# Optimization experiments

Measured on AMD Instinct MI355X. Metric: run time of the kernel, lower is better.

## Reference

```python
import math
import jax, jax.numpy as jnp
import numpy as np

B, L, ENC_IN, TFEAT = 32, 1024, 21, 4
DM, EXP = 256, 2
DI = DM * EXP            # 512 d_inner
DST = 64                 # d_state (= configs.d_ff in this repo)
HD = 64                  # headdim
NH = DI // HD            # 8 heads
DC = 4                   # d_conv
NL = 4                   # n_layers
PRED = 192
CO = 21
Q = 64                   # SSD chunk length
DIP = 2 * DI + 2 * DST + NH    # in_proj out dim (z, xBC, dt)
CONVD = DI + 2 * DST           # depthwise-conv channels


def silu(x):
    return x * jax.nn.sigmoid(x)


def positional_embedding(l, d):
    pe = np.zeros((l, d), np.float32)
    pos = np.arange(l, dtype=np.float32)[:, None]
    div = np.exp(np.arange(0, d, 2, dtype=np.float32) * (-math.log(10000.0) / d))
    pe[:, 0::2] = np.sin(pos * div)
    pe[:, 1::2] = np.cos(pos * div)
    return jnp.asarray(pe)


def layernorm(x, g, b):
    m = jnp.mean(x, -1, keepdims=True)
    v = jnp.mean((x - m) ** 2, -1, keepdims=True)
    return (x - m) * jax.lax.rsqrt(v + 1e-5) * g + b


def segsum(x):
    # x: (..., T) -> (..., T, T); out[i,j] = sum_{j<k<=i} x[k], -inf above diagonal
    T = x.shape[-1]
    xx = jnp.broadcast_to(x[..., :, None], (*x.shape, T))
    m1 = jnp.tril(jnp.ones((T, T), bool), -1)
    xs = jnp.cumsum(jnp.where(m1, xx, 0.0), axis=-2)
    m2 = jnp.tril(jnp.ones((T, T), bool), 0)
    return jnp.where(m2, xs, -jnp.inf)


def ssd(X, A, Bm, Cm):
    # chunked SSD (Mamba2). X: (b,l,h,p) = x*dt; A: (b,l,h) = dt*(-exp(A_log)); B,C: (b,l,n)
    b, l, h, p = X.shape
    c = l // Q
    Xc = X.reshape(b, c, Q, h, p)
    Ac = A.reshape(b, c, Q, h).transpose(0, 3, 1, 2)      # (b,h,c,q)
    Bc = Bm.reshape(b, c, Q, -1)
    Cc = Cm.reshape(b, c, Q, -1)
    Acum = jnp.cumsum(Ac, -1)                              # (b,h,c,q)
    Lmat = jnp.exp(segsum(Ac))                             # (b,h,c,q,q)
    Y_diag = jnp.einsum('bcqn,bcsn,bhcqs,bcshp->bcqhp', Cc, Bc, Lmat, Xc)
    decay_states = jnp.exp(Acum[..., -1:] - Acum)          # (b,h,c,q)
    states = jnp.einsum('bcqn,bhcq,bcqhp->bchpn', Bc, decay_states, Xc)
    states = jnp.concatenate([jnp.zeros_like(states[:, :1]), states], axis=1)  # (b,c+1,h,p,n)
    decay_chunk = jnp.exp(segsum(jnp.pad(Acum[..., -1], ((0, 0), (0, 0), (1, 0)))))  # (b,h,c+1,c+1)
    new_states = jnp.einsum('bhzc,bchpn->bzhpn', decay_chunk, states)
    states = new_states[:, :-1]                            # (b,c,h,p,n) entering each chunk
    sdo = jnp.exp(Acum)                                    # (b,h,c,q)
    Y_off = jnp.einsum('bcqn,bchpn,bhcq->bcqhp', Cc, states, sdo)
    return (Y_diag + Y_off).reshape(b, l, h, p)


def mamba2(x, Wi, cw, cb, dtb, Alog, Dp, gw, Wo):
    b, l, _ = x.shape
    zxbcdt = x @ Wi.T                                      # (b,l,DIP)
    z = zxbcdt[..., :DI]
    xBC = zxbcdt[..., DI:DI + CONVD]
    dt = zxbcdt[..., DI + CONVD:]
    # causal depthwise conv (kernel DC) + SiLU
    xp = jnp.pad(xBC, ((0, 0), (DC - 1, 0), (0, 0)))
    xBC = silu(sum(xp[:, k:k + l, :] * cw[:, k] for k in range(DC)) + cb)
    xs = xBC[..., :DI].reshape(b, l, NH, HD)
    Bm = xBC[..., DI:DI + DST]
    Cm = xBC[..., DI + DST:]
    dt = jax.nn.softplus(dt + dtb)                         # (b,l,NH)
    A = -jnp.exp(Alog)                                     # (NH,)
    y = ssd(xs * dt[..., None], dt * A, Bm, Cm) + xs * Dp[:, None]
    y = y.reshape(b, l, DI)
    y = y * silu(z)                                        # gated RMSNorm
    y = y * jax.lax.rsqrt(jnp.mean(y * y, -1, keepdims=True) + 1e-5) * gw
    return y @ Wo.T


def setup_inputs():
    key = jax.random.key(0)
    ks = jax.random.split(key, 16)
    x_enc = jax.random.normal(ks[0], (B, L, ENC_IN), jnp.float32)
    x_mark_enc = jax.random.normal(ks[1], (B, L, TFEAT), jnp.float32)
    x_dec = jax.random.normal(ks[2], (B, 240, ENC_IN), jnp.float32)
    x_mark_dec = jax.random.normal(ks[3], (B, 240, TFEAT), jnp.float32)
    token_w = jax.random.normal(ks[4], (DM, ENC_IN, 3), jnp.float32) * 0.1
    temb_w = jax.random.normal(ks[5], (DM, TFEAT), jnp.float32) * 0.1
    ln_g = jnp.ones((NL, DM), jnp.float32)
    ln_b = jnp.zeros((NL, DM), jnp.float32)
    in_proj_w = jax.random.normal(ks[6], (NL, DIP, DM), jnp.float32) * (DM ** -0.5)
    conv_w = jax.random.normal(ks[7], (NL, CONVD, DC), jnp.float32) * 0.2
    conv_b = jnp.zeros((NL, CONVD), jnp.float32)
    dt_bias = jax.random.normal(ks[8], (NL, NH), jnp.float32) * 0.5
    A_log = jnp.log(jax.random.uniform(ks[9], (NL, NH), jnp.float32, 1.0, 16.0))
    Dskip = jnp.ones((NL, NH), jnp.float32)
    gnorm_w = jnp.ones((NL, DI), jnp.float32)
    out_proj_w = jax.random.normal(ks[10], (NL, DM, DI), jnp.float32) * (DI ** -0.5)
    head_w = jax.random.normal(ks[11], (CO, DM), jnp.float32) * (DM ** -0.5)
    return dict(x_enc=x_enc, x_mark_enc=x_mark_enc, x_dec=x_dec, x_mark_dec=x_mark_dec,
                token_w=token_w, temb_w=temb_w, ln_g=ln_g, ln_b=ln_b,
                in_proj_w=in_proj_w, conv_w=conv_w, conv_b=conv_b, dt_bias=dt_bias,
                A_log=A_log, Dskip=Dskip, gnorm_w=gnorm_w, out_proj_w=out_proj_w,
                head_w=head_w)


def reference(x_enc, x_mark_enc, x_dec, x_mark_dec, token_w, temb_w, ln_g, ln_b,
              in_proj_w, conv_w, conv_b, dt_bias, A_log, Dskip, gnorm_w, out_proj_w, head_w):
    # instance normalization (detached stats)
    mean = jax.lax.stop_gradient(jnp.mean(x_enc, 1, keepdims=True))
    xz = x_enc - mean
    std = jax.lax.stop_gradient(jnp.sqrt(jnp.var(xz, axis=1, keepdims=True) + 1e-5))
    xz = xz / std
    l = xz.shape[1]
    # token embedding: circular-pad Conv1d(enc_in->d_model, k=3)
    xpad = jnp.pad(xz, ((0, 0), (1, 1), (0, 0)), mode='wrap')
    tok = sum(jnp.einsum('blc,dc->bld', xpad[:, k:k + l], token_w[:, :, k]) for k in range(3))
    h = tok + positional_embedding(l, DM)[None] + x_mark_enc @ temb_w.T
    for i in range(NL):
        y = mamba2(h, in_proj_w[i], conv_w[i], conv_b[i], dt_bias[i], A_log[i],
                   Dskip[i], gnorm_w[i], out_proj_w[i])
        h = layernorm(h + y, ln_g[i], ln_b[i])
    out = h @ head_w.T
    out = out * std + mean
    return out[:, -PRED:, :]
```

## Files before the change

### kernel.cpp

```cpp
#include <hip/hip_runtime.h>
#include <hip/hip_bf16.h>


typedef unsigned short ushort_t;
typedef unsigned int uint_t;
typedef __attribute__((ext_vector_type(8))) short short8;
typedef __attribute__((ext_vector_type(4))) float f32x4;
typedef __attribute__((ext_vector_type(4))) ushort_t ushort4_t;

__device__ __forceinline__ float b2f(ushort_t u) {
    uint_t v = ((uint_t)u) << 16;
    return __builtin_bit_cast(float, v);
}
__device__ __forceinline__ ushort_t f2b(float f) {
    uint_t u = __builtin_bit_cast(uint_t, f);
    uint_t r = (u + 0x7FFFu + ((u >> 16) & 1u)) >> 16;
    return (ushort_t)r;
}
__device__ __forceinline__ uint_t cvt_pk2(float a, float b) {
    uint_t r;
    asm("v_cvt_pk_bf16_f32 %0, %1, %2" : "=v"(r) : "v"(a), "v"(b));
    return r;
}
__device__ __forceinline__ float silu_f(float x) {
    return x / (1.f + __expf(-x));
}
__device__ __forceinline__ void gl_lds16(const ushort_t* g, ushort_t* l) {
    __builtin_amdgcn_global_load_lds(
        (const __attribute__((address_space(1))) unsigned int*)g,
        (__attribute__((address_space(3))) unsigned int*)l, 16, 0, 0);
}

__global__ __launch_bounds__(256) void cvt_pad_ip(const float* __restrict__ in,
        ushort_t* __restrict__ out) {
    int i = blockIdx.x * 256 + threadIdx.x;
    if (i >= 4 * 1280 * 256) return;
    int layer = i / (1280 * 256);
    int rem = i - layer * 1280 * 256;
    int n = rem >> 8, k = rem & 255;
    out[i] = (n < 1160) ? f2b(in[(size_t)layer * 1160 * 256 + n * 256 + k]) : (ushort_t)0;
}
__global__ __launch_bounds__(256) void cvt_wop(const float* __restrict__ in,
        const float* __restrict__ gw, ushort_t* __restrict__ out) {
    int i = blockIdx.x * 256 + threadIdx.x;
    int layer = i >> 17;
    int c = i & 511;
    out[i] = f2b(in[i] * gw[layer * 512 + c]);
}
__global__ __launch_bounds__(256) void cvt_convw(const float* __restrict__ in,
        float* __restrict__ out) {
    int i = blockIdx.x * 256 + threadIdx.x;
    if (i >= 10240) return;
    int layer = i / 2560;
    int rem = i - layer * 2560;
    int k = rem / 640, ch = rem - k * 640;
    out[i] = in[layer * 2560 + ch * 4 + k];
}

__global__ __launch_bounds__(256) void pe_kernel(float* __restrict__ pe) {
    int l = blockIdx.x, d = threadIdx.x;
    float div = __expf((float)(d & ~1) * (-9.210340371976184f / 256.0f));
    float arg = (float)l * div;
    pe[l * 256 + d] = (d & 1) ? cosf(arg) : sinf(arg);
}

__global__ __launch_bounds__(256) void stats_kernel(const float* __restrict__ xe,
        float* __restrict__ meanb, float* __restrict__ stdb, float* __restrict__ rstdb) {
    int bi = blockIdx.x;
    int b = bi / 21, c = bi - b * 21;
    int tid = threadIdx.x;
    float s = 0.f, s2 = 0.f;
    for (int l = tid; l < 1024; l += 256) {
        float v = xe[(b * 1024 + l) * 21 + c];
        s += v; s2 += v * v;
    }
    __shared__ float r1[4], r2[4];
    for (int o = 32; o > 0; o >>= 1) { s += __shfl_down(s, o, 64); s2 += __shfl_down(s2, o, 64); }
    if ((tid & 63) == 0) { r1[tid >> 6] = s; r2[tid >> 6] = s2; }
    __syncthreads();
    if (tid == 0) {
        float S = r1[0] + r1[1] + r1[2] + r1[3];
        float S2 = r2[0] + r2[1] + r2[2] + r2[3];
        float m = S * (1.f / 1024.f);
        float var = S2 * (1.f / 1024.f) - m * m;
        float sd = sqrtf(var + 1e-5f);
        meanb[bi] = m; stdb[bi] = sd; rstdb[bi] = 1.f / sd;
    }
}

__global__ __launch_bounds__(256) void embed3_kernel(const float* __restrict__ xe,
        const float* __restrict__ xm, const float* __restrict__ tokw,
        const float* __restrict__ tembw, const float* __restrict__ pe,
        const float* __restrict__ meanb, const float* __restrict__ rstdb,
        float* __restrict__ h, ushort_t* __restrict__ hbf) {
    int blk = blockIdx.x;
    int b = blk >> 4, t = blk & 15;
    int l0 = t * 64;
    int tid = threadIdx.x;
    __shared__ float xw[66][22];
    __shared__ float xmw[64][4];
    __shared__ float mn[21], rs[21];
    if (tid < 21) { mn[tid] = meanb[b * 21 + tid]; rs[tid] = rstdb[b * 21 + tid]; }
    float twr[63];
    {
        const float* tp = tokw + tid * 63;
        #pragma unroll
        for (int i = 0; i < 63; i++) twr[i] = tp[i];
    }
    float tbr[4];
    #pragma unroll
    for (int k = 0; k < 4; k++) tbr[k] = tembw[tid * 4 + k];
    __syncthreads();
    for (int i = tid; i < 1386; i += 256) {
        int row = i / 21, c = i - row * 21;
        int gl = (l0 - 1 + row + 1024) & 1023;
        xw[row][c] = (xe[(size_t)(b * 1024 + gl) * 21 + c] - mn[c]) * rs[c];
    }
    {
        int row = tid >> 2, c = tid & 3;
        xmw[row][c] = xm[(size_t)(b * 1024 + l0 + row) * 4 + c];
    }
    __syncthreads();
    int d = tid;
    float acc2 = 0.f, acc1 = 0.f;
    for (int r = 0; r < 66; r++) {
        float s0 = 0.f, s1 = 0.f, s2 = 0.f;
        #pragma unroll
        for (int c = 0; c < 21; c++) {
            float xv = xw[r][c];
            s0 += xv * twr[c * 3 + 0];
            s1 += xv * twr[c * 3 + 1];
            s2 += xv * twr[c * 3 + 2];
        }
        if (r >= 2) {
            int li = r - 2;
            float acc = acc2 + s2 + pe[(size_t)(l0 + li) * 256 + d];
            #pragma unroll
            for (int k = 0; k < 4; k++) acc += xmw[li][k] * tbr[k];
            size_t o = (size_t)(b * 1024 + l0 + li) * 256 + d;
            h[o] = acc;
            hbf[o] = f2b(acc);
        }
        acc2 = acc1 + s1;
        acc1 = s0;
    }
}

template<int KDIM>
__device__ __forceinline__ void gemm128_main(const ushort_t* __restrict__ Ab,
        const ushort_t* __restrict__ Wb, ushort_t* sA, ushort_t* sW,
        f32x4 (&acc)[16], int m0, int n0) {
    int tid = threadIdx.x;
    int w = tid >> 6, lane = tid & 63;
    int wm = w >> 1, wn = w & 1;
    int rr = lane & 15, quad = lane >> 4;
    int srow0 = w * 32 + (lane >> 2);
    int skk = (lane & 3) * 8;
    int sl0 = w * 1024 + lane * 8;
    for (int k0 = 0; k0 < KDIM; k0 += 64) {
        __syncthreads();
        #pragma unroll
        for (int p = 0; p < 2; p++) {
            #pragma unroll
            for (int j = 0; j < 2; j++) {
                int row = srow0 + j * 16;
                int koff = k0 + p * 32 + skk;
                gl_lds16(Ab + (size_t)(m0 + row) * KDIM + koff, &sA[p * 4096 + sl0 + j * 512]);
                gl_lds16(Wb + (size_t)(n0 + row) * KDIM + koff, &sW[p * 4096 + sl0 + j * 512]);
            }
        }
        __syncthreads();
        #pragma unroll
        for (int p = 0; p < 2; p++) {
            short8 a[4], b[4];
            #pragma unroll
            for (int i = 0; i < 4; i++)
                a[i] = *(const short8*)&sA[p * 4096 + (wm * 64 + i * 16 + rr) * 32 + quad * 8];
            #pragma unroll
            for (int j = 0; j < 4; j++)
                b[j] = *(const short8*)&sW[p * 4096 + (wn * 64 + j * 16 + rr) * 32 + quad * 8];
            #pragma unroll
            for (int i = 0; i < 4; i++)
                #pragma unroll
                for (int j = 0; j < 4; j++)
                    acc[i * 4 + j] = __builtin_amdgcn_mfma_f32_16x16x32_bf16(a[i], b[j], acc[i * 4 + j], 0, 0, 0);
        }
    }
}

__global__ __launch_bounds__(256) void gemm_ip(const ushort_t* __restrict__ A,
        const ushort_t* __restrict__ W, ushort_t* __restrict__ zbuf,
        ushort_t* __restrict__ xbuf) {
    int g = blockIdx.x;
    int xcd = g & 7, s = g >> 3;
    int sq = s / 10;
    int tn = s - sq * 10;
    int tm = (sq << 3) | xcd;
    int m0 = tm * 128, n0 = tn * 128;
    __shared__ ushort_t sA[8192], sW[8192];
    f32x4 acc[16];
    #pragma unroll
    for (int i = 0; i < 16; i++) acc[i] = (f32x4){0.f, 0.f, 0.f, 0.f};
    gemm128_main<256>(A, W, sA, sW, acc, m0, n0);
    int lane = threadIdx.x & 63, w = threadIdx.x >> 6;
    int wm = w >> 1, wn = w & 1;
    int rr = lane & 15, quad = lane >> 4;
    #pragma unroll
    for (int i = 0; i < 4; i++) {
        int mrow = m0 + wm * 64 + i * 16 + quad * 4;
        #pragma unroll
        for (int j = 0; j < 4; j++) {
            int n = n0 + wn * 64 + j * 16 + rr;
            uint_t u01 = cvt_pk2(acc[i * 4 + j][0], acc[i * 4 + j][1]);
            uint_t u23 = cvt_pk2(acc[i * 4 + j][2], acc[i * 4 + j][3]);
            ushort_t vs[4] = {(ushort_t)u01, (ushort_t)(u01 >> 16),
                              (ushort_t)u23, (ushort_t)(u23 >> 16)};
            #pragma unroll
            for (int r2 = 0; r2 < 4; r2++) {
                if (n < 512) zbuf[(size_t)(mrow + r2) * 512 + n] = vs[r2];
                else if (n < 1160) xbuf[(size_t)(mrow + r2) * 704 + (n - 512)] = vs[r2];
            }
        }
    }
}

__global__ __launch_bounds__(256) void gemm_og(const ushort_t* __restrict__ Yb,
        const ushort_t* __restrict__ Zb, const ushort_t* __restrict__ Wb,
        float* __restrict__ h, ushort_t* __restrict__ hbf,
        const float* __restrict__ lng, const float* __restrict__ lnb) {
    int m0 = blockIdx.x * 64;
    int tid = threadIdx.x;
    int w = tid >> 6, lane = tid & 63;
    int wm = w >> 1, wn = w & 1;
    int rr = lane & 15, quad = lane >> 4;
    __shared__ ushort_t sA[4096];
    __shared__ ushort_t sW[16384];
    __shared__ float gssq[64];
    __shared__ float rsum[64][2], rssq[64][2];

    int arow = tid >> 2;
    int akq = (tid & 3) * 16;
    const ushort_t* yrow = Yb + (size_t)(m0 + arow) * 512 + akq;
    const ushort_t* zrow = Zb + (size_t)(m0 + arow) * 512 + akq;
    ushort_t* adst = &sA[((tid & 3) >> 1) * 2048 + arow * 32 + (tid & 1) * 16];

    f32x4 acc[2][8];
    #pragma unroll
    for (int i = 0; i < 2; i++)
        #pragma unroll
        for (int j = 0; j < 8; j++) acc[i][j] = (f32x4){0.f, 0.f, 0.f, 0.f};
    float ssqr = 0.f;

    short8 y0 = *(const short8*)(yrow);
    short8 y1 = *(const short8*)(yrow + 8);
    short8 z0 = *(const short8*)(zrow);
    short8 z1 = *(const short8*)(zrow + 8);

    for (int k0 = 0; k0 < 512; k0 += 64) {
        __syncthreads();
        short8 ga, gb;
        {
            uint_t* gau = (uint_t*)&ga;
            uint_t* gbu = (uint_t*)&gb;
            #pragma unroll
            for (int jj = 0; jj < 8; jj += 2) {
                float g0 = b2f(((ushort_t*)&y0)[jj]) * silu_f(b2f(((ushort_t*)&z0)[jj]));
                float g1 = b2f(((ushort_t*)&y0)[jj + 1]) * silu_f(b2f(((ushort_t*)&z0)[jj + 1]));
                ssqr += g0 * g0 + g1 * g1;
                gau[jj >> 1] = cvt_pk2(g0, g1);
            }
            #pragma unroll
            for (int jj = 0; jj < 8; jj += 2) {
                float g0 = b2f(((ushort_t*)&y1)[jj]) * silu_f(b2f(((ushort_t*)&z1)[jj]));
                float g1 = b2f(((ushort_t*)&y1)[jj + 1]) * silu_f(b2f(((ushort_t*)&z1)[jj + 1]));
                ssqr += g0 * g0 + g1 * g1;
                gbu[jj >> 1] = cvt_pk2(g0, g1);
            }
        }
        *(short8*)adst = ga;
        *(short8*)(adst + 8) = gb;
        if (k0 + 64 < 512) {
            y0 = *(const short8*)(yrow + k0 + 64);
            y1 = *(const short8*)(yrow + k0 + 72);
            z0 = *(const short8*)(zrow + k0 + 64);
            z1 = *(const short8*)(zrow + k0 + 72);
        }
        #pragma unroll
        for (int p = 0; p < 2; p++) {
            #pragma unroll
            for (int j = 0; j < 4; j++)
                gl_lds16(Wb + (size_t)(w * 64 + j * 16 + (lane >> 2)) * 512
                             + k0 + p * 32 + (lane & 3) * 8,
                         &sW[p * 8192 + w * 2048 + j * 512 + lane * 8]);
        }
        __syncthreads();
        #pragma unroll
        for (int p = 0; p < 2; p++) {
            short8 a[2], b[8];
            #pragma unroll
            for (int i = 0; i < 2; i++)
                a[i] = *(const short8*)&sA[p * 2048 + (wm * 32 + i * 16 + rr) * 32 + quad * 8];
            #pragma unroll
            for (int j = 0; j < 8; j++)
                b[j] = *(const short8*)&sW[p * 8192 + (wn * 128 + j * 16 + rr) * 32 + quad * 8];
            #pragma unroll
            for (int i = 0; i < 2; i++)
                #pragma unroll
                for (int j = 0; j < 8; j++)
                    acc[i][j] = __builtin_amdgcn_mfma_f32_16x16x32_bf16(a[i], b[j], acc[i][j], 0, 0, 0);
        }
    }

    ssqr += __shfl_xor(ssqr, 1, 64);
    ssqr += __shfl_xor(ssqr, 2, 64);
    if ((tid & 3) == 0) gssq[arow] = ssqr;
    __syncthreads();

    float gl[8], bl[8];
    #pragma unroll
    for (int j = 0; j < 8; j++) {
        int col = wn * 128 + j * 16 + rr;
        gl[j] = lng[col]; bl[j] = lnb[col];
    }
    #pragma unroll
    for (int i = 0; i < 2; i++) {
        #pragma unroll
        for (int r2 = 0; r2 < 4; r2++) {
            int rowl = wm * 32 + i * 16 + quad * 4 + r2;
            float rmsv = rsqrtf(gssq[rowl] * (1.f / 512.f) + 1e-5f);
            size_t gbase = (size_t)(m0 + rowl) * 256;
            float s = 0.f, s2 = 0.f;
            #pragma unroll
            for (int j = 0; j < 8; j++) {
                int col = wn * 128 + j * 16 + rr;
                float xv = h[gbase + col] + acc[i][j][r2] * rmsv;
                acc[i][j][r2] = xv;
                s += xv; s2 += xv * xv;
            }
            #pragma unroll
            for (int o = 1; o < 16; o <<= 1) {
                s += __shfl_xor(s, o, 64);
                s2 += __shfl_xor(s2, o, 64);
            }
            if (rr == 0) { rsum[rowl][wn] = s; rssq[rowl][wn] = s2; }
        }
    }
    __syncthreads();
    #pragma unroll
    for (int i = 0; i < 2; i++) {
        #pragma unroll
        for (int r2 = 0; r2 < 4; r2++) {
            int rowl = wm * 32 + i * 16 + quad * 4 + r2;
            float S = rsum[rowl][0] + rsum[rowl][1];
            float S2 = rssq[rowl][0] + rssq[rowl][1];
            float mu = S * (1.f / 256.f);
            float var = S2 * (1.f / 256.f) - mu * mu;
            float rstd = rsqrtf(var + 1e-5f);
            size_t gbase = (size_t)(m0 + rowl) * 256;
            #pragma unroll
            for (int j = 0; j < 8; j++) {
                int col = wn * 128 + j * 16 + rr;
                float o = (acc[i][j][r2] - mu) * rstd * gl[j] + bl[j];
                h[gbase + col] = o;
                hbf[gbase + col] = f2b(o);
            }
        }
    }
}

__global__ __launch_bounds__(256) void conv_kernel(const ushort_t* __restrict__ xbuf,
        const float* __restrict__ cwt, const float* __restrict__ cb,
        const float* __restrict__ dtb, ushort_t* __restrict__ xc,
        float* __restrict__ dts) {
    if (blockIdx.x >= 2560) {
        int r = (blockIdx.x - 2560) * 256 + threadIdx.x;
        short8 dv = *(const short8*)(xbuf + (size_t)r * 704 + 640);
        #pragma unroll
        for (int j = 0; j < 8; j++) {
            float x = b2f(((ushort_t*)&dv)[j]) + dtb[j];
            dts[(size_t)r * 8 + j] = (x > 20.f) ? x : log1pf(__expf(x));
        }
        return;
    }
    int idx = blockIdx.x * 256 + threadIdx.x;
    int g = idx % 80;
    int rt = idx / 80;
    int ch0 = g * 8;
    int b = rt >> 8;
    int l0 = (rt & 255) << 2;
    float wgt[4][8];
    #pragma unroll
    for (int k = 0; k < 4; k++) {
        float4 w0 = *(const float4*)(cwt + k * 640 + ch0);
        float4 w1 = *(const float4*)(cwt + k * 640 + ch0 + 4);
        wgt[k][0] = w0.x; wgt[k][1] = w0.y; wgt[k][2] = w0.z; wgt[k][3] = w0.w;
        wgt[k][4] = w1.x; wgt[k][5] = w1.y; wgt[k][6] = w1.z; wgt[k][7] = w1.w;
    }
    float bias[8];
    {
        float4 b0 = *(const float4*)(cb + ch0);
        float4 b1 = *(const float4*)(cb + ch0 + 4);
        bias[0] = b0.x; bias[1] = b0.y; bias[2] = b0.z; bias[3] = b0.w;
        bias[4] = b1.x; bias[5] = b1.y; bias[6] = b1.z; bias[7] = b1.w;
    }
    short8 xr[7];
    const ushort_t* base = xbuf + (size_t)(b * 1024 + l0) * 704 + ch0;
    #pragma unroll
    for (int i = 0; i < 7; i++) {
        int ll = l0 - 3 + i;
        if (ll >= 0) xr[i] = *(const short8*)(base + (ptrdiff_t)(i - 3) * 704);
        else         xr[i] = (short8){0, 0, 0, 0, 0, 0, 0, 0};
    }
    #pragma unroll
    for (int lo = 0; lo < 4; lo++) {
        float acc[8];
        #pragma unroll
        for (int j = 0; j < 8; j++) acc[j] = bias[j];
        #pragma unroll
        for (int k = 0; k < 4; k++) {
            #pragma unroll
            for (int j = 0; j < 8; j++)
                acc[j] += b2f(((ushort_t*)&xr[lo + k])[j]) * wgt[k][j];
        }
        short8 o;
        #pragma unroll
        for (int j = 0; j < 8; j++) ((ushort_t*)&o)[j] = f2b(silu_f(acc[j]));
        *(short8*)(xc + (size_t)(b * 1024 + l0 + lo) * 640 + ch0) = o;
    }
}

__global__ __launch_bounds__(256) void ssd_stateA4(const ushort_t* __restrict__ xc,
        const float* __restrict__ dts, const float* __restrict__ alog,
        float* __restrict__ stbuf, float* __restrict__ acbuf) {
    int idx = blockIdx.x;
    int bh = idx >> 2, grp = idx & 3;
    int b = bh >> 3, h = bh & 7;
    float Ah = -__expf(alog[h]);
    int tid = threadIdx.x;
    int q = tid >> 2, pb = (tid & 3) * 16;
    int w = tid >> 6, lane = tid & 63;
    int rr = lane & 15, quad = lane >> 4, qb = w * 16;

    __shared__ ushort_t Bt[64][68], Xt[64][68];
    __shared__ float dec_s[64];
    __shared__ float ad_sh;

    float T[4][4];
    #pragma unroll
    for (int t = 0; t < 4; t++)
        #pragma unroll
        for (int r2 = 0; r2 < 4; r2++) T[t][r2] = 0.f;

    ushort_t bv[16], xv[16];
    float d_pf = 0.f;
    {
        int chunk = grp * 4;
        int l0 = chunk * 64;
        const ushort_t* xrow = xc + (size_t)(b * 1024 + l0 + q) * 640;
        *(short8*)&bv[0] = *(const short8*)(xrow + 512 + pb);
        *(short8*)&bv[8] = *(const short8*)(xrow + 512 + pb + 8);
        *(short8*)&xv[0] = *(const short8*)(xrow + h * 64 + pb);
        *(short8*)&xv[8] = *(const short8*)(xrow + h * 64 + pb + 8);
        if (tid < 64)
            d_pf = dts[(size_t)(b * 1024 + l0 + tid) * 8 + h];
    }

    for (int c4 = 0; c4 < 4; c4++) {
        int chunk = grp * 4 + c4;
        size_t cidx = (size_t)bh * 16 + chunk;
        #pragma unroll
        for (int j = 0; j < 16; j++) Xt[pb + j][q] = xv[j];
        if (tid < 64) {
            float d = d_pf;
            float a = d * Ah;
            #pragma unroll
            for (int off = 1; off < 64; off <<= 1) {
                float t = __shfl_up(a, off, 64);
                if (tid >= off) a += t;
            }
            acbuf[cidx * 64 + tid] = a;
            float tot = __shfl(a, 63, 64);
            dec_s[tid] = __expf(tot - a) * d;
            if (tid == 0) ad_sh = __expf(tot);
        }
        __syncthreads();
        {
            float dq = dec_s[q];
            #pragma unroll
            for (int j = 0; j < 16; j += 2) {
                uint_t u = cvt_pk2(b2f(bv[j]) * dq, b2f(bv[j + 1]) * dq);
                Bt[pb + j][q] = (ushort_t)u;
                Bt[pb + j + 1][q] = (ushort_t)(u >> 16);
            }
        }
        if (c4 < 3) {
            int l0n = (chunk + 1) * 64;
            const ushort_t* xrow = xc + (size_t)(b * 1024 + l0n + q) * 640;
            *(short8*)&bv[0] = *(const short8*)(xrow + 512 + pb);
            *(short8*)&bv[8] = *(const short8*)(xrow + 512 + pb + 8);
            *(short8*)&xv[0] = *(const short8*)(xrow + h * 64 + pb);
            *(short8*)&xv[8] = *(const short8*)(xrow + h * 64 + pb + 8);
            if (tid < 64)
                d_pf = dts[(size_t)(b * 1024 + l0n + tid) * 8 + h];
        }
        __syncthreads();
        f32x4 acc[4];
        #pragma unroll
        for (int t = 0; t < 4; t++) acc[t] = (f32x4){0.f, 0.f, 0.f, 0.f};
        #pragma unroll
        for (int ks = 0; ks < 2; ks++) {
            short8 a = *(const short8*)(&Bt[qb + rr][ks * 32 + quad * 8]);
            #pragma unroll
            for (int t = 0; t < 4; t++) {
                short8 bb = *(const short8*)(&Xt[t * 16 + rr][ks * 32 + quad * 8]);
                acc[t] = __builtin_amdgcn_mfma_f32_16x16x32_bf16(a, bb, acc[t], 0, 0, 0);
            }
        }
        {
            float ad = ad_sh;
            #pragma unroll
            for (int t = 0; t < 4; t++)
                #pragma unroll
                for (int r2 = 0; r2 < 4; r2++)
                    T[t][r2] = ad * T[t][r2] + acc[t][r2];
        }
        __syncthreads();
    }
    float* sb = stbuf + (size_t)idx * 4096;
    #pragma unroll
    for (int t = 0; t < 4; t++) {
        int p = t * 16 + rr;
        #pragma unroll
        for (int r2 = 0; r2 < 4; r2++)
            sb[(qb + quad * 4 + r2) * 64 + p] = T[t][r2];
    }
}

__global__ __launch_bounds__(256) void ssd_outBC4(const ushort_t* __restrict__ xc,
        const float* __restrict__ dts, const float* __restrict__ acbuf,
        const float* __restrict__ dsk, const float* __restrict__ stbuf,
        ushort_t* __restrict__ ybuf) {
    int idx = blockIdx.x;
    int bh = idx >> 2, grp = idx & 3;
    int b = bh >> 3, h = bh & 7;
    float Dh = dsk[h];
    int tid = threadIdx.x;
    int q = tid >> 2, pb = (tid & 3) * 16;
    int w = tid >> 6, lane = tid & 63;
    int rr = lane & 15, quad = lane >> 4, qb = w * 16;

    __shared__ ushort_t Cs[64][68], Bs[64][68], Xt[64][68],
                        Bt[64][68], Shi[64][68], Slo[64][68];
    ushort_t (&Gs)[64][68] = Bs;
    __shared__ float acum_s[64], dtq_s[64], ea_s[64], dec_s[64];
    __shared__ float ad_sh;

    float S[4][4];
    #pragma unroll
    for (int t = 0; t < 4; t++)
        #pragma unroll
        for (int r2 = 0; r2 < 4; r2++) S[t][r2] = 0.f;
    for (int g = 0; g < grp; g++) {
        float Ag = 1.f;
        #pragma unroll
        for (int c = 0; c < 4; c++)
            Ag *= __expf(acbuf[((size_t)bh * 16 + g * 4 + c) * 64 + 63]);
        const float* s0 = stbuf + (size_t)(bh * 4 + g) * 4096;
        #pragma unroll
        for (int t = 0; t < 4; t++) {
            int p = t * 16 + rr;
            #pragma unroll
            for (int r2 = 0; r2 < 4; r2++)
                S[t][r2] = Ag * S[t][r2] + s0[(qb + quad * 4 + r2) * 64 + p];
        }
    }

    ushort_t bv[16], cv[16], xv[16];
    float a_pf = 0.f, d_pf = 0.f;
    {
        int chunk = grp * 4;
        int l0 = chunk * 64;
        const ushort_t* xrow = xc + (size_t)(b * 1024 + l0 + q) * 640;
        *(short8*)&bv[0] = *(const short8*)(xrow + 512 + pb);
        *(short8*)&bv[8] = *(const short8*)(xrow + 512 + pb + 8);
        *(short8*)&cv[0] = *(const short8*)(xrow + 576 + pb);
        *(short8*)&cv[8] = *(const short8*)(xrow + 576 + pb + 8);
        *(short8*)&xv[0] = *(const short8*)(xrow + h * 64 + pb);
        *(short8*)&xv[8] = *(const short8*)(xrow + h * 64 + pb + 8);
        if (tid < 64) {
            size_t cidx = (size_t)bh * 16 + chunk;
            a_pf = acbuf[cidx * 64 + tid];
            d_pf = dts[(size_t)(b * 1024 + l0 + tid) * 8 + h];
        }
    }

    int qq0 = qb + quad * 4;
    for (int c4 = 0; c4 < 4; c4++) {
        int chunk = grp * 4 + c4;
        int l0 = chunk * 64;
        *(short8*)&Bs[q][pb]     = *(const short8*)&bv[0];
        *(short8*)&Bs[q][pb + 8] = *(const short8*)&bv[8];
        *(short8*)&Cs[q][pb]     = *(const short8*)&cv[0];
        *(short8*)&Cs[q][pb + 8] = *(const short8*)&cv[8];
        #pragma unroll
        for (int j = 0; j < 16; j++) Xt[pb + j][q] = xv[j];
        if (tid < 64) {
            float a = a_pf;
            acum_s[tid] = a;
            ea_s[tid] = __expf(a);
            float d = d_pf;
            dtq_s[tid] = d;
            float tot = __shfl(a, 63, 64);
            dec_s[tid] = __expf(tot - a) * d;
            if (tid == 0) ad_sh = __expf(tot);
        }
        #pragma unroll
        for (int t = 0; t < 4; t++) {
            int p = t * 16 + rr;
            uint_t h01 = cvt_pk2(S[t][0], S[t][1]);
            uint_t h23 = cvt_pk2(S[t][2], S[t][3]);
            float l0r = S[t][0] - b2f((ushort_t)h01);
            float l1r = S[t][1] - b2f((ushort_t)(h01 >> 16));
            float l2r = S[t][2] - b2f((ushort_t)h23);
            float l3r = S[t][3] - b2f((ushort_t)(h23 >> 16));
            uint_t lo01 = cvt_pk2(l0r, l1r);
            uint_t lo23 = cvt_pk2(l2r, l3r);
            *(uint2*)&Shi[p][qq0] = make_uint2(h01, h23);
            *(uint2*)&Slo[p][qq0] = make_uint2(lo01, lo23);
        }
        __syncthreads();

        {
            float dq = dec_s[q];
            #pragma unroll
            for (int j = 0; j < 16; j += 2) {
                uint_t u = cvt_pk2(b2f(bv[j]) * dq, b2f(bv[j + 1]) * dq);
                Bt[pb + j][q] = (ushort_t)u;
                Bt[pb + j + 1][q] = (ushort_t)(u >> 16);
            }
        }
        if (c4 < 3) {
            int l0n = (chunk + 1) * 64;
            const ushort_t* xrow = xc + (size_t)(b * 1024 + l0n + q) * 640;
            *(short8*)&bv[0] = *(const short8*)(xrow + 512 + pb);
            *(short8*)&bv[8] = *(const short8*)(xrow + 512 + pb + 8);
            *(short8*)&cv[0] = *(const short8*)(xrow + 576 + pb);
            *(short8*)&cv[8] = *(const short8*)(xrow + 576 + pb + 8);
            *(short8*)&xv[0] = *(const short8*)(xrow + h * 64 + pb);
            *(short8*)&xv[8] = *(const short8*)(xrow + h * 64 + pb + 8);
            if (tid < 64) {
                size_t cidxn = (size_t)bh * 16 + chunk + 1;
                a_pf = acbuf[cidxn * 64 + tid];
                d_pf = dts[(size_t)(b * 1024 + l0n + tid) * 8 + h];
            }
        }
        uint_t gp01[4], gp23[4];
        {
            f32x4 g[4];
            #pragma unroll
            for (int t = 0; t < 4; t++) g[t] = (f32x4){0.f, 0.f, 0.f, 0.f};
            #pragma unroll
            for (int ks = 0; ks < 2; ks++) {
                short8 a = *(const short8*)(&Cs[qb + rr][ks * 32 + quad * 8]);
                #pragma unroll
                for (int t = 0; t < 4; t++) {
                    short8 bb = *(const short8*)(&Bs[t * 16 + rr][ks * 32 + quad * 8]);
                    g[t] = __builtin_amdgcn_mfma_f32_16x16x32_bf16(a, bb, g[t], 0, 0, 0);
                }
            }
            #pragma unroll
            for (int t = 0; t < 4; t++) {
                int s = t * 16 + rr;
                float as = acum_s[s], dss = dtq_s[s];
                float vv[4];
                #pragma unroll
                for (int r2 = 0; r2 < 4; r2++) {
                    int qq = qq0 + r2;
                    vv[r2] = (s <= qq) ? g[t][r2] * __expf(acum_s[qq] - as) * dss : 0.f;
                }
                gp01[t] = cvt_pk2(vv[0], vv[1]);
                gp23[t] = cvt_pk2(vv[2], vv[3]);
            }
        }
        __syncthreads();
        #pragma unroll
        for (int t = 0; t < 4; t++) {
            int s = t * 16 + rr;
            Gs[qq0][s]     = (ushort_t)gp01[t];
            Gs[qq0 + 1][s] = (ushort_t)(gp01[t] >> 16);
            Gs[qq0 + 2][s] = (ushort_t)gp23[t];
            Gs[qq0 + 3][s] = (ushort_t)(gp23[t] >> 16);
        }
        __syncthreads();

        f32x4 aD[4], aO[4];
        #pragma unroll
        for (int t = 0; t < 4; t++) { aD[t] = (f32x4){0.f,0.f,0.f,0.f}; aO[t] = (f32x4){0.f,0.f,0.f,0.f}; }
        #pragma unroll
        for (int ks = 0; ks < 2; ks++) {
            short8 ga = *(const short8*)(&Gs[qb + rr][ks * 32 + quad * 8]);
            short8 ca = *(const short8*)(&Cs[qb + rr][ks * 32 + quad * 8]);
            #pragma unroll
            for (int t = 0; t < 4; t++) {
                short8 xb = *(const short8*)(&Xt[t * 16 + rr][ks * 32 + quad * 8]);
                short8 sh = *(const short8*)(&Shi[t * 16 + rr][ks * 32 + quad * 8]);
                short8 sl = *(const short8*)(&Slo[t * 16 + rr][ks * 32 + quad * 8]);
                aD[t] = __builtin_amdgcn_mfma_f32_16x16x32_bf16(ga, xb, aD[t], 0, 0, 0);
                aO[t] = __builtin_amdgcn_mfma_f32_16x16x32_bf16(ca, sh, aO[t], 0, 0, 0);
                aO[t] = __builtin_amdgcn_mfma_f32_16x16x32_bf16(ca, sl, aO[t], 0, 0, 0);
            }
        }
        {
            f32x4 acc[4];
            #pragma unroll
            for (int t = 0; t < 4; t++) acc[t] = (f32x4){0.f, 0.f, 0.f, 0.f};
            #pragma unroll
            for (int ks = 0; ks < 2; ks++) {
                short8 a = *(const short8*)(&Bt[qb + rr][ks * 32 + quad * 8]);
                #pragma unroll
                for (int t = 0; t < 4; t++) {
                    short8 bb = *(const short8*)(&Xt[t * 16 + rr][ks * 32 + quad * 8]);
                    acc[t] = __builtin_amdgcn_mfma_f32_16x16x32_bf16(a, bb, acc[t], 0, 0, 0);
                }
            }
            #pragma unroll
            for (int t = 0; t < 4; t++) {
                int p = t * 16 + rr;
                float yv[4];
                #pragma unroll
                for (int r2 = 0; r2 < 4; r2++) {
                    int qq = qq0 + r2;
                    yv[r2] = aD[t][r2] + ea_s[qq] * aO[t][r2] + Dh * b2f(Xt[p][qq]);
                }
                uint_t u01 = cvt_pk2(yv[0], yv[1]);
                uint_t u23 = cvt_pk2(yv[2], yv[3]);
                size_t base = (size_t)(b * 1024 + l0 + qq0) * 512 + h * 64 + p;
                ybuf[base]        = (ushort_t)u01;
                ybuf[base + 512]  = (ushort_t)(u01 >> 16);
                ybuf[base + 1024] = (ushort_t)u23;
                ybuf[base + 1536] = (ushort_t)(u23 >> 16);
            }
            float ad = ad_sh;
            #pragma unroll
            for (int t = 0; t < 4; t++)
                #pragma unroll
                for (int r2 = 0; r2 < 4; r2++)
                    S[t][r2] = ad * S[t][r2] + acc[t][r2];
        }
        __syncthreads();
    }
}

__global__ __launch_bounds__(256) void head_kernel(const float* __restrict__ h,
        const float* __restrict__ hw, const float* __restrict__ stdb,
        const float* __restrict__ meanb, float* __restrict__ out) {
    int blk = blockIdx.x;
    int b = blk / 192, t = blk - b * 192;
    int l = 832 + t;
    int tid = threadIdx.x;
    __shared__ float hr[256];
    hr[tid] = h[(size_t)(b * 1024 + l) * 256 + tid];
    __syncthreads();
    if (tid < 21) {
        float acc = 0.f;
        for (int k = 0; k < 256; k++) acc += hr[k] * hw[tid * 256 + k];
        out[(size_t)blk * 21 + tid] = acc * stdb[b * 21 + tid] + meanb[b * 21 + tid];
    }
}

extern "C" void kernel_launch(void* const* d_in, const int* in_sizes, int n_in,
                              void* d_out, int out_size, void* d_ws, size_t ws_size,
                              hipStream_t stream) {
    const float* x_enc  = (const float*)d_in[0];
    const float* x_mark = (const float*)d_in[1];
    const float* tokw   = (const float*)d_in[4];
    const float* tembw  = (const float*)d_in[5];
    const float* ln_g   = (const float*)d_in[6];
    const float* ln_b   = (const float*)d_in[7];
    const float* ipw    = (const float*)d_in[8];
    const float* cw     = (const float*)d_in[9];
    const float* cb     = (const float*)d_in[10];
    const float* dtb    = (const float*)d_in[11];
    const float* alog   = (const float*)d_in[12];
    const float* dsk    = (const float*)d_in[13];
    const float* gw     = (const float*)d_in[14];
    const float* opw    = (const float*)d_in[15];
    const float* hw     = (const float*)d_in[16];
    float* out = (float*)d_out;

    char* w = (char*)d_ws;
    size_t off = 0;
    auto alloc = [&](size_t bytes) -> void* {
        void* p = w + off;
        off += (bytes + 255) & ~(size_t)255;
        return p;
    };
    float* meanb  = (float*)alloc(672 * 4);
    float* stdb   = (float*)alloc(672 * 4);
    float* rstdb  = (float*)alloc(672 * 4);
    float* dts    = (float*)alloc((size_t)262144 * 4);
    float* pebuf  = (float*)alloc((size_t)262144 * 4);
    float* cwt    = (float*)alloc((size_t)10240 * 4);
    float* hbuf   = (float*)alloc((size_t)8388608 * 4);
    ushort_t* hbf = (ushort_t*)alloc((size_t)8388608 * 2);
    ushort_t* zbuf= (ushort_t*)alloc((size_t)32768 * 512 * 2);
    ushort_t* xc  = (ushort_t*)alloc((size_t)32768 * 640 * 2);
    char* R       = (char*)alloc((size_t)71303168);
    ushort_t* ybuf= (ushort_t*)alloc((size_t)32768 * 512 * 2);
    ushort_t* wipb= (ushort_t*)alloc((size_t)4 * 1280 * 256 * 2);
    ushort_t* wopb= (ushort_t*)alloc((size_t)4 * 256 * 512 * 2);
    ushort_t* xbuf = (ushort_t*)R;
    float* stbuf   = (float*)R;
    float* acbuf   = (float*)(R + 67108864);
    (void)ws_size; (void)in_sizes; (void)n_in; (void)out_size;

    stats_kernel<<<672, 256, 0, stream>>>(x_enc, meanb, stdb, rstdb);
    pe_kernel<<<1024, 256, 0, stream>>>(pebuf);
    cvt_pad_ip<<<5120, 256, 0, stream>>>(ipw, wipb);
    cvt_wop<<<2048, 256, 0, stream>>>(opw, gw, wopb);
    cvt_convw<<<40, 256, 0, stream>>>(cw, cwt);
    embed3_kernel<<<512, 256, 0, stream>>>(x_enc, x_mark, tokw, tembw, pebuf,
                                           meanb, rstdb, hbuf, hbf);

    for (int layer = 0; layer < 4; layer++) {
        gemm_ip<<<2560, 256, 0, stream>>>(hbf, wipb + (size_t)layer * 1280 * 256,
                                          zbuf, xbuf);
        conv_kernel<<<2688, 256, 0, stream>>>(xbuf, cwt + layer * 2560,
                                              cb + layer * 640, dtb + layer * 8,
                                              xc, dts);
        ssd_stateA4<<<1024, 256, 0, stream>>>(xc, dts, alog + layer * 8, stbuf, acbuf);
        ssd_outBC4<<<1024, 256, 0, stream>>>(xc, dts, acbuf, dsk + layer * 8,
                                             stbuf, ybuf);
        gemm_og<<<512, 256, 0, stream>>>(ybuf, zbuf,
                                         wopb + (size_t)layer * 256 * 512,
                                         hbuf, hbf,
                                         ln_g + layer * 256, ln_b + layer * 256);
    }

    head_kernel<<<6144, 256, 0, stream>>>(hbuf, hw, stdb, meanb, out);
}
```

Before: 741.3 us.

## Fuse SiLU gating and RMS sum-of-squares into SSD output kernel; shrink out-proj tile

Moves the y*silu(z) gating and the per-row sum-of-squares for the gated RMSNorm from the out-projection GEMM prologue into the SSD output kernel. That kernel writes the gated value plus per-head partial sums, which the GEMM reads and adds. The out-projection GEMM then streams its A operand directly to LDS with async loads, uses 32-row tiles, and launches twice as many blocks. This removes the z read and elementwise work from the GEMM's critical loop and improves occupancy. The cost is extra z loads, shuffles and a small ssq buffer in the SSD kernel, and the gated value is rounded to bf16 before the GEMM, as before.

After: 788.0 us. 1.06x slower.

```diff
diff --git a/kernel.cpp b/kernel.cpp
--- a/kernel.cpp
+++ b/kernel.cpp
@@ -224,67 +224,31 @@
     }
 }
 
-__global__ __launch_bounds__(256) void gemm_og(const ushort_t* __restrict__ Yb,
-        const ushort_t* __restrict__ Zb, const ushort_t* __restrict__ Wb,
+__global__ __launch_bounds__(256) void gemm_og(const ushort_t* __restrict__ Gb,
+        const float* __restrict__ ssqb, const ushort_t* __restrict__ Wb,
         float* __restrict__ h, ushort_t* __restrict__ hbf,
         const float* __restrict__ lng, const float* __restrict__ lnb) {
-    int m0 = blockIdx.x * 64;
+    int m0 = blockIdx.x * 32;
     int tid = threadIdx.x;
     int w = tid >> 6, lane = tid & 63;
     int wm = w >> 1, wn = w & 1;
     int rr = lane & 15, quad = lane >> 4;
-    __shared__ ushort_t sA[4096];
+    __shared__ ushort_t sA[2048];
     __shared__ ushort_t sW[16384];
-    __shared__ float gssq[64];
-    __shared__ float rsum[64][2], rssq[64][2];
-
-    int arow = tid >> 2;
-    int akq = (tid & 3) * 16;
-    const ushort_t* yrow = Yb + (size_t)(m0 + arow) * 512 + akq;
-    const ushort_t* zrow = Zb + (size_t)(m0 + arow) * 512 + akq;
-    ushort_t* adst = &sA[((tid & 3) >> 1) * 2048 + arow * 32 + (tid & 1) * 16];
-
-    f32x4 acc[2][8];
-    #pragma unroll
-    for (int i = 0; i < 2; i++)
-        #pragma unroll
-        for (int j = 0; j < 8; j++) acc[i][j] = (f32x4){0.f, 0.f, 0.f, 0.f};
-    float ssqr = 0.f;
-
-    short8 y0 = *(const short8*)(yrow);
-    short8 y1 = *(const short8*)(yrow + 8);
-    short8 z0 = *(const short8*)(zrow);
-    short8 z1 = *(const short8*)(zrow + 8);
+    __shared__ float rsum[32][2], rssq[32][2];
+
+    f32x4 acc[8];
+    #pragma unroll
+    for (int j = 0; j < 8; j++) acc[j] = (f32x4){0.f, 0.f, 0.f, 0.f};
+
+    int ap = w >> 1;
+    int arow = ((w & 1) << 4) + (lane >> 2);
+    const ushort_t* agp = Gb + (size_t)(m0 + arow) * 512 + ap * 32 + (lane & 3) * 8;
+    ushort_t* adst = &sA[ap * 1024 + ((w & 1) << 9) + lane * 8];
 
     for (int k0 = 0; k0 < 512; k0 += 64) {
         __syncthreads();
-        short8 ga, gb;
-        {
-            uint_t* gau = (uint_t*)&ga;
-            uint_t* gbu = (uint_t*)&gb;
-            #pragma unroll
-            for (int jj = 0; jj < 8; jj += 2) {
-                float g0 = b2f(((ushort_t*)&y0)[jj]) * silu_f(b2f(((ushort_t*)&z0)[jj]));
-                float g1 = b2f(((ushort_t*)&y0)[jj + 1]) * silu_f(b2f(((ushort_t*)&z0)[jj + 1]));
-                ssqr += g0 * g0 + g1 * g1;
-                gau[jj >> 1] = cvt_pk2(g0, g1);
-            }
-            #pragma unroll
-            for (int jj = 0; jj < 8; jj += 2) {
-                float g0 = b2f(((ushort_t*)&y1)[jj]) * silu_f(b2f(((ushort_t*)&z1)[jj]));
-                float g1 = b2f(((ushort_t*)&y1)[jj + 1]) * silu_f(b2f(((ushort_t*)&z1)[jj + 1]));
-                ssqr += g0 * g0 + g1 * g1;
-                gbu[jj >> 1] = cvt_pk2(g0, g1);
-            }
-        }
-        *(short8*)adst = ga;
-        *(short8*)(adst + 8) = gb;
-        if (k0 + 64 < 512) {
-            y0 = *(const short8*)(yrow + k0 + 64);
-            y1 = *(const short8*)(yrow + k0 + 72);
-            z0 = *(const short8*)(zrow + k0 + 64);
-            z1 = *(const short8*)(zrow + k0 + 72);
-        }
+        gl_lds16(agp + k0, adst);
         #pragma unroll
         for (int p = 0; p < 2; p++) {
             #pragma unroll
@@ -296,25 +260,14 @@
         __syncthreads();
         #pragma unroll
         for (int p = 0; p < 2; p++) {
-            short8 a[2], b[8];
-            #pragma unroll
-            for (int i = 0; i < 2; i++)
-                a[i] = *(const short8*)&sA[p * 2048 + (wm * 32 + i * 16 + rr) * 32 + quad * 8];
-            #pragma unroll
-            for (int j = 0; j < 8; j++)
-                b[j] = *(const short8*)&sW[p * 8192 + (wn * 128 + j * 16 + rr) * 32 + quad * 8];
-            #pragma unroll
-            for (int i = 0; i < 2; i++)
-                #pragma unroll
-                for (int j = 0; j < 8; j++)
-                    acc[i][j] = __builtin_amdgcn_mfma_f32_16x16x32_bf16(a[i], b[j], acc[i][j], 0, 0, 0);
-        }
-    }
-
-    ssqr += __shfl_xor(ssqr, 1, 64);
-    ssqr += __shfl_xor(ssqr, 2, 64);
-    if ((tid & 3) == 0) gssq[arow] = ssqr;
-    __syncthreads();
+            short8 a = *(const short8*)&sA[p * 1024 + (wm * 16 + rr) * 32 + quad * 8];
+            #pragma unroll
+            for (int j = 0; j < 8; j++) {
+                short8 bv = *(const short8*)&sW[p * 8192 + (wn * 128 + j * 16 + rr) * 32 + quad * 8];
+                acc[j] = __builtin_amdgcn_mfma_f32_16x16x32_bf16(a, bv, acc[j], 0, 0, 0);
+            }
+        }
+    }
 
     float gl[8], bl[8];
     #pragma unroll
@@ -323,47 +276,45 @@
         gl[j] = lng[col]; bl[j] = lnb[col];
     }
     #pragma unroll
-    for (int i = 0; i < 2; i++) {
-        #pragma unroll
-        for (int r2 = 0; r2 < 4; r2++) {
-            int rowl = wm * 32 + i * 16 + quad * 4 + r2;
-            float rmsv = rsqrtf(gssq[rowl] * (1.f / 512.f) + 1e-5f);
-            size_t gbase = (size_t)(m0 + rowl) * 256;
-            float s = 0.f, s2 = 0.f;
-            #pragma unroll
-            for (int j = 0; j < 8; j++) {
-                int col = wn * 128 + j * 16 + rr;
-                float xv = h[gbase + col] + acc[i][j][r2] * rmsv;
-                acc[i][j][r2] = xv;
-                s += xv; s2 += xv * xv;
-            }
-            #pragma unroll
-            for (int o = 1; o < 16; o <<= 1) {
-                s += __shfl_xor(s, o, 64);
-                s2 += __shfl_xor(s2, o, 64);
-            }
-            if (rr == 0) { rsum[rowl][wn] = s; rssq[rowl][wn] = s2; }
-        }
+    for (int r2 = 0; r2 < 4; r2++) {
+        int rowl = wm * 16 + quad * 4 + r2;
+        const float* sq = ssqb + (size_t)(m0 + rowl) * 8;
+        float4 q0 = *(const float4*)sq;
+        float4 q1 = *(const float4*)(sq + 4);
+        float ss = q0.x + q0.y + q0.z + q0.w + q1.x + q1.y + q1.z + q1.w;
+        float rmsv = rsqrtf(ss * (1.f / 512.f) + 1e-5f);
+        size_t gbase = (size_t)(m0 + rowl) * 256;
+        float s = 0.f, s2 = 0.f;
+        #pragma unroll
+        for (int j = 0; j < 8; j++) {
+            int col = wn * 128 + j * 16 + rr;
+            float xv = h[gbase + col] + acc[j][r2] * rmsv;
+            acc[j][r2] = xv;
+            s += xv; s2 += xv * xv;
+        }
+        #pragma unroll
+        for (int o = 1; o < 16; o <<= 1) {
+            s += __shfl_xor(s, o, 64);
+            s2 += __shfl_xor(s2, o, 64);
+        }
+        if (rr == 0) { rsum[rowl][wn] = s; rssq[rowl][wn] = s2; }
     }
     __syncthreads();
     #pragma unroll
-    for (int i = 0; i < 2; i++) {
-        #pragma unroll
-        for (int r2 = 0; r2 < 4; r2++) {
-            int rowl = wm * 32 + i * 16 + quad * 4 + r2;
-            float S = rsum[rowl][0] + rsum[rowl][1];
-            float S2 = rssq[rowl][0] + rssq[rowl][1];
-            float mu = S * (1.f / 256.f);
-            float var = S2 * (1.f / 256.f) - mu * mu;
-            float rstd = rsqrtf(var + 1e-5f);
-            size_t gbase = (size_t)(m0 + rowl) * 256;
-            #pragma unroll
-            for (int j = 0; j < 8; j++) {
-                int col = wn * 128 + j * 16 + rr;
-                float o = (acc[i][j][r2] - mu) * rstd * gl[j] + bl[j];
-                h[gbase + col] = o;
-                hbf[gbase + col] = f2b(o);
-            }
+    for (int r2 = 0; r2 < 4; r2++) {
+        int rowl = wm * 16 + quad * 4 + r2;
+        float S = rsum[rowl][0] + rsum[rowl][1];
+        float S2 = rssq[rowl][0] + rssq[rowl][1];
+        float mu = S * (1.f / 256.f);
+        float var = S2 * (1.f / 256.f) - mu * mu;
+        float rstd = rsqrtf(var + 1e-5f);
+        size_t gbase = (size_t)(m0 + rowl) * 256;
+        #pragma unroll
+        for (int j = 0; j < 8; j++) {
+            int col = wn * 128 + j * 16 + rr;
+            float o = (acc[j][r2] - mu) * rstd * gl[j] + bl[j];
+            h[gbase + col] = o;
+            hbf[gbase + col] = f2b(o);
         }
     }
 }
@@ -539,7 +490,8 @@
 __global__ __launch_bounds__(256) void ssd_outBC4(const ushort_t* __restrict__ xc,
         const float* __restrict__ dts, const float* __restrict__ acbuf,
         const float* __restrict__ dsk, const float* __restrict__ stbuf,
-        ushort_t* __restrict__ ybuf) {
+        const ushort_t* __restrict__ Zb, ushort_t* __restrict__ ybuf,
+        float* __restrict__ ssqb) {
     int idx = blockIdx.x;
     int bh = idx >> 2, grp = idx & 3;
     int b = bh >> 3, h = bh & 7;
@@ -598,6 +550,15 @@
     for (int c4 = 0; c4 < 4; c4++) {
         int chunk = grp * 4 + c4;
         int l0 = chunk * 64;
+        ushort_t zg[4][4];
+        {
+            const ushort_t* zb0 = Zb + (size_t)(b * 1024 + l0 + qq0) * 512 + h * 64 + rr;
+            #pragma unroll
+            for (int t = 0; t < 4; t++)
+                #pragma unroll
+                for (int r2 = 0; r2 < 4; r2++)
+                    zg[t][r2] = zb0[(size_t)r2 * 512 + t * 16];
+        }
         *(short8*)&Bs[q][pb]     = *(const short8*)&bv[0];
         *(short8*)&Bs[q][pb + 8] = *(const short8*)&bv[8];
         *(short8*)&Cs[q][pb]     = *(const short8*)&cv[0];
@@ -723,22 +684,40 @@
                     acc[t] = __builtin_amdgcn_mfma_f32_16x16x32_bf16(a, bb, acc[t], 0, 0, 0);
                 }
             }
+            float sp[4] = {0.f, 0.f, 0.f, 0.f};
             #pragma unroll
             for (int t = 0; t < 4; t++) {
                 int p = t * 16 + rr;
-                float yv[4];
+                float gv[4];
                 #pragma unroll
                 for (int r2 = 0; r2 < 4; r2++) {
                     int qq = qq0 + r2;
-                    yv[r2] = aD[t][r2] + ea_s[qq] * aO[t][r2] + Dh * b2f(Xt[p][qq]);
+                    float yv = aD[t][r2] + ea_s[qq] * aO[t][r2] + Dh * b2f(Xt[p][qq]);
+                    float g = yv * silu_f(b2f(zg[t][r2]));
+                    gv[r2] = g;
+                    sp[r2] += g * g;
                 }
-                uint_t u01 = cvt_pk2(yv[0], yv[1]);
-                uint_t u23 = cvt_pk2(yv[2], yv[3]);
+                uint_t u01 = cvt_pk2(gv[0], gv[1]);
+                uint_t u23 = cvt_pk2(gv[2], gv[3]);
                 size_t base = (size_t)(b * 1024 + l0 + qq0) * 512 + h * 64 + p;
                 ybuf[base]        = (ushort_t)u01;
                 ybuf[base + 512]  = (ushort_t)(u01 >> 16);
                 ybuf[base + 1024] = (ushort_t)u23;
                 ybuf[base + 1536] = (ushort_t)(u23 >> 16);
+            }
+            #pragma unroll
+            for (int o = 1; o < 16; o <<= 1) {
+                sp[0] += __shfl_xor(sp[0], o, 64);
+                sp[1] += __shfl_xor(sp[1], o, 64);
+                sp[2] += __shfl_xor(sp[2], o, 64);
+                sp[3] += __shfl_xor(sp[3], o, 64);
+            }
+            if (rr == 0) {
+                size_t rbase = (size_t)(b * 1024 + l0 + qq0) * 8 + h;
+                ssqb[rbase]      = sp[0];
+                ssqb[rbase + 8]  = sp[1];
+                ssqb[rbase + 16] = sp[2];
+                ssqb[rbase + 24] = sp[3];
             }
             float ad = ad_sh;
             #pragma unroll
@@ -801,6 +780,7 @@
     float* dts    = (float*)alloc((size_t)262144 * 4);
     float* pebuf  = (float*)alloc((size_t)262144 * 4);
     float* cwt    = (float*)alloc((size_t)10240 * 4);
+    float* ssqb   = (float*)alloc((size_t)262144 * 4);
     float* hbuf   = (float*)alloc((size_t)8388608 * 4);
     ushort_t* hbf = (ushort_t*)alloc((size_t)8388608 * 2);
     ushort_t* zbuf= (ushort_t*)alloc((size_t)32768 * 512 * 2);
@@ -830,11 +810,11 @@
                                               xc, dts);
         ssd_stateA4<<<1024, 256, 0, stream>>>(xc, dts, alog + layer * 8, stbuf, acbuf);
         ssd_outBC4<<<1024, 256, 0, stream>>>(xc, dts, acbuf, dsk + layer * 8,
-                                             stbuf, ybuf);
-        gemm_og<<<512, 256, 0, stream>>>(ybuf, zbuf,
-                                         wopb + (size_t)layer * 256 * 512,
-                                         hbuf, hbf,
-                                         ln_g + layer * 256, ln_b + layer * 256);
+                                             stbuf, zbuf, ybuf, ssqb);
+        gemm_og<<<1024, 256, 0, stream>>>(ybuf, ssqb,
+                                          wopb + (size_t)layer * 256 * 512,
+                                          hbuf, hbf,
+                                          ln_g + layer * 256, ln_b + layer * 256);
     }
 
     head_kernel<<<6144, 256, 0, stream>>>(hbuf, hw, stdb, meanb, out);
```
